# Kernel tuning notes

Measured on AMD Instinct MI355X. Metric: run time of the kernel, lower is better.

The kernel has to match this reference:

```python
import jax, jax.numpy as jnp
import numpy as np

B, L, C, H = 4, 4096, 1024, 16


def setup_inputs() -> dict:
    key = jax.random.key(0)
    k1, k2, k3 = jax.random.split(key, 3)
    x = jax.random.normal(k1, (B, L, C), dtype=jnp.float32)
    # torch nn.Linear params: weight (out, in), bias (out,)
    W_qkv = jax.random.normal(k2, (3 * C, C), dtype=jnp.float32) * 0.02
    b_qkv = jnp.zeros((3 * C,), dtype=jnp.float32)
    W_out = jax.random.normal(k3, (C, C), dtype=jnp.float32) * 0.02
    b_out = jnp.zeros((C,), dtype=jnp.float32)
    return {"x": x, "W_qkv": W_qkv, "b_qkv": b_qkv, "W_out": W_out,
            "b_out": b_out, "num_heads": H}


def reference(x, W_qkv, b_qkv, W_out, b_out, num_heads):
    # Faithful to the source, INCLUDING its head-axis bug:
    # q,k,v stay (B, L, H, D); attention is computed over the HEAD axis
    # (H x H per token), and the final transpose(1,2).reshape scrambles
    # sequence/head layout exactly as torch does.
    b, l, c = x.shape
    h = num_heads
    d = c // h
    scale = d ** (-0.5)
    qkv = (x @ W_qkv.T + b_qkv).reshape(b, l, 3, h, d)
    q, k, v = qkv[:, :, 0], qkv[:, :, 1], qkv[:, :, 2]  # (B, L, H, D)
    # (B,L,H,D) @ (B,L,D,H) -> (B,L,H,H)
    attn = jnp.einsum('blhd,blgd->blhg', q, k) * scale
    attn = jax.nn.softmax(attn, axis=-1)
    # dropout is identity in eval mode
    out = jnp.einsum('blhg,blgd->blhd', attn, v)      # (B, L, H, D)
    out = jnp.swapaxes(out, 1, 2).reshape(b, l, c)    # torch transpose(1,2).reshape
    return out @ W_out.T + b_out
```

## Files before the change

kernel.cpp:

```cpp
#include <hip/hip_runtime.h>
#include <hip/hip_bf16.h>


typedef __attribute__((ext_vector_type(8))) short bf16x8;
typedef __attribute__((ext_vector_type(4))) float f32x4;

__device__ __forceinline__ float bf2f(unsigned short u) {
    union { unsigned int i; float f; } x;
    x.i = ((unsigned int)u) << 16;
    return x.f;
}
__device__ __forceinline__ unsigned short f2bf(float f) {
    unsigned int u = __float_as_uint(f);
    u = (u + 0x7FFFu + ((u >> 16) & 1u)) >> 16;
    return (unsigned short)u;
}

#define VMCNT4() asm volatile("s_waitcnt vmcnt(4)" ::: "memory")
#define VMCNT0() asm volatile("s_waitcnt vmcnt(0)" ::: "memory")
#define LGKM0()  asm volatile("s_waitcnt lgkmcnt(0)" ::: "memory")
#define BAR()    __builtin_amdgcn_s_barrier()

__global__ __launch_bounds__(256) void cast_all(const float* __restrict__ x,
                                                const float* __restrict__ wq,
                                                const float* __restrict__ wo,
                                                unsigned short* __restrict__ xb,
                                                unsigned short* __restrict__ wqb,
                                                unsigned short* __restrict__ wob) {
    const size_t base = (size_t)blockIdx.x * 2048 + threadIdx.x;
#pragma unroll
    for (int it = 0; it < 8; ++it) {
        size_t i = base + (size_t)it * 256;
        const float4* s; ushort4* d; size_t off;
        if (i < 4194304)      { s = (const float4*)x;  d = (ushort4*)xb;  off = i; }
        else if (i < 4980736) { s = (const float4*)wq; d = (ushort4*)wqb; off = i - 4194304; }
        else                  { s = (const float4*)wo; d = (ushort4*)wob; off = i - 4980736; }
        float4 v = s[off];
        ushort4 o;
        o.x = f2bf(v.x); o.y = f2bf(v.y); o.z = f2bf(v.z); o.w = f2bf(v.w);
        d[off] = o;
    }
}

template<int OUTF32>
__global__ __launch_bounds__(512, 2) void gemm256(const unsigned short* __restrict__ A,
                                                  const unsigned short* __restrict__ B,
                                                  const float* __restrict__ bias,
                                                  unsigned short* __restrict__ Cb,
                                                  float* __restrict__ Cf,
                                                  int M, int N, int K, int NXT) {
    __shared__ __align__(16) unsigned short lds[2][2][2][8192];

    const int tid  = threadIdx.x;
    const int lane = tid & 63;
    const int wave = tid >> 6;
    const int wr = wave >> 2;
    const int wc = wave & 3;
    const int fr = lane & 15;
    const int fq = lane >> 4;
    const int frx = fr & 7;

    const int nwg  = gridDim.x;
    const int orig = blockIdx.x;
    const int wg   = (orig & 7) * (nwg >> 3) + (orig >> 3);
    const int tileM = (wg / NXT) * 256;
    const int tileN = (wg % NXT) * 256;

    const int r8  = tid >> 3;
    const int jsw = (tid & 7) ^ (r8 & 7);
    const unsigned short* Ap = A;
    const unsigned short* Bp = B;

#define STAGE(nb, OPp, HH, ktt) do {                                                   \
    const unsigned short* gb = (OPp) ? Bp : Ap;                                        \
    const int rb = ((OPp) ? tileN : tileM) + (HH) * 128 + r8;                          \
    const unsigned short* s0 = gb + (size_t)rb * K + (ktt) * 64 + jsw * 8;             \
    unsigned short* d0 = &lds[nb][OPp][HH][tid * 8];                                   \
    __builtin_amdgcn_global_load_lds((const __attribute__((address_space(1))) void*)s0,\
        (__attribute__((address_space(3))) void*)d0, 16, 0, 0);                        \
    __builtin_amdgcn_global_load_lds(                                                  \
        (const __attribute__((address_space(1))) void*)(s0 + (size_t)64 * K),          \
        (__attribute__((address_space(3))) void*)(d0 + 4096), 16, 0, 0);               \
} while (0)

#define READ_A(h) do {                                                                 \
    _Pragma("unroll") for (int i2 = 0; i2 < 4; ++i2) {                                 \
        const int ar = (wr * 64 + i2 * 16 + fr) * 64;                                  \
        af[i2][0] = *(const bf16x8*)&lds[cur][0][h][ar + ((fq ^ frx) << 3)];           \
        af[i2][1] = *(const bf16x8*)&lds[cur][0][h][ar + (((4 + fq) ^ frx) << 3)];     \
    }                                                                                  \
} while (0)

#define READ_B(g) do {                                                                 \
    _Pragma("unroll") for (int j2 = 0; j2 < 2; ++j2) {                                 \
        const int br = (wc * 32 + j2 * 16 + fr) * 64;                                  \
        bfr[2*(g)+j2][0] = *(const bf16x8*)&lds[cur][1][g][br + ((fq ^ frx) << 3)];    \
        bfr[2*(g)+j2][1] = *(const bf16x8*)&lds[cur][1][g][br + (((4 + fq) ^ frx) << 3)];\
    }                                                                                  \
} while (0)

#define MFMA_Q(h, g) do {                                                              \
    __builtin_amdgcn_s_setprio(1);                                                     \
    _Pragma("unroll") for (int i2 = 0; i2 < 4; ++i2)                                   \
    _Pragma("unroll") for (int j2 = 0; j2 < 2; ++j2) {                                 \
        acc[(h)*4+i2][(g)*2+j2] = __builtin_amdgcn_mfma_f32_16x16x32_bf16(             \
            af[i2][0], bfr[2*(g)+j2][0], acc[(h)*4+i2][(g)*2+j2], 0, 0, 0);            \
        acc[(h)*4+i2][(g)*2+j2] = __builtin_amdgcn_mfma_f32_16x16x32_bf16(             \
            af[i2][1], bfr[2*(g)+j2][1], acc[(h)*4+i2][(g)*2+j2], 0, 0, 0);            \
    }                                                                                  \
    __builtin_amdgcn_s_setprio(0);                                                     \
} while (0)

    f32x4 acc[8][4];
#pragma unroll
    for (int i = 0; i < 8; ++i)
#pragma unroll
        for (int j = 0; j < 4; ++j) acc[i][j] = (f32x4){0.f, 0.f, 0.f, 0.f};

    STAGE(0, 0, 0, 0);
    STAGE(0, 1, 0, 0);
    STAGE(0, 1, 1, 0);
    STAGE(0, 0, 1, 0);
    VMCNT4();
    BAR();

    const int NT = K >> 6;
    int cur = 0;
    for (int kt = 0; kt < NT - 1; ++kt) {
        const int nb = cur ^ 1;
        bf16x8 af[4][2], bfr[4][2];
        READ_A(0); READ_B(0); STAGE(nb, 0, 0, kt + 1); VMCNT4(); BAR(); LGKM0(); MFMA_Q(0, 0);
        READ_B(1); STAGE(nb, 1, 0, kt + 1); VMCNT4(); BAR(); LGKM0(); MFMA_Q(0, 1);
        READ_A(1); STAGE(nb, 1, 1, kt + 1); BAR(); LGKM0(); MFMA_Q(1, 0);
        STAGE(nb, 0, 1, kt + 1); VMCNT4(); BAR(); MFMA_Q(1, 1);
        cur = nb;
    }
    VMCNT0();
    BAR();
    {
        bf16x8 af[4][2], bfr[4][2];
        READ_A(0); READ_B(0); LGKM0(); MFMA_Q(0, 0);
        READ_B(1);            LGKM0(); MFMA_Q(0, 1);
        READ_A(1);            LGKM0(); MFMA_Q(1, 0);
                                       MFMA_Q(1, 1);
    }

#pragma unroll
    for (int i = 0; i < 8; ++i) {
        const int row = tileM + (i >> 2) * 128 + wr * 64 + (i & 3) * 16 + fq * 4;
#pragma unroll
        for (int j = 0; j < 4; ++j) {
            const int col = tileN + (j >> 1) * 128 + wc * 32 + (j & 1) * 16 + fr;
            const float bv = bias[col];
#pragma unroll
            for (int r = 0; r < 4; ++r) {
                const float v = acc[i][j][r] + bv;
                if (OUTF32) Cf[(size_t)(row + r) * N + col] = v;
                else        Cb[(size_t)(row + r) * N + col] = f2bf(v);
            }
        }
    }
#undef STAGE
#undef READ_A
#undef READ_B
#undef MFMA_Q
}

__global__ __launch_bounds__(256) void attn_kernel(const unsigned short* __restrict__ qkv,
                                                   unsigned short* __restrict__ scr) {
    __shared__ __align__(16) unsigned short sbuf[4][3072];
    __shared__ float Pl[4][256];

    const int wave = threadIdx.x >> 6, lane = threadIdx.x & 63;
    const int token = blockIdx.x * 4 + wave;
    const int b = token >> 12, l = token & 4095;

    const unsigned short* src = qkv + (size_t)token * 3072;
#pragma unroll
    for (int i = 0; i < 6; ++i) {
        int off = (i * 64 + lane) * 8;
        *(bf16x8*)&sbuf[wave][off] = *(const bf16x8*)&src[off];
    }
    __syncthreads();

    const unsigned short* sq = sbuf[wave];

    float sv[4];
#pragma unroll
    for (int r = 0; r < 4; ++r) {
        const int p = r * 64 + lane;
        const int h = p >> 4, g = p & 15;
        float acc = 0.f;
#pragma unroll
        for (int d8 = 0; d8 < 8; ++d8) {
            bf16x8 qa = *(const bf16x8*)&sq[h * 64 + d8 * 8];
            bf16x8 kb = *(const bf16x8*)&sq[1024 + g * 64 + d8 * 8];
#pragma unroll
            for (int j = 0; j < 8; ++j)
                acc += bf2f((unsigned short)qa[j]) * bf2f((unsigned short)kb[j]);
        }
        sv[r] = acc * 0.125f;
    }

#pragma unroll
    for (int r = 0; r < 4; ++r) {
        float m = sv[r];
        m = fmaxf(m, __shfl_xor(m, 1));
        m = fmaxf(m, __shfl_xor(m, 2));
        m = fmaxf(m, __shfl_xor(m, 4));
        m = fmaxf(m, __shfl_xor(m, 8));
        float e = __expf(sv[r] - m);
        float s = e;
        s += __shfl_xor(s, 1);
        s += __shfl_xor(s, 2);
        s += __shfl_xor(s, 4);
        s += __shfl_xor(s, 8);
        Pl[wave][r * 64 + lane] = e / s;
    }
    __syncthreads();

    float vreg[16];
#pragma unroll
    for (int g = 0; g < 16; ++g) vreg[g] = bf2f(sq[2048 + g * 64 + lane]);

    const int q_ = l >> 4, j = l & 15;
    const size_t base = ((size_t)b * 4096 + q_) * 1024 + j * 64 + lane;
#pragma unroll
    for (int h = 0; h < 16; ++h) {
        float acc = 0.f;
#pragma unroll
        for (int g = 0; g < 16; ++g) acc += Pl[wave][h * 16 + g] * vreg[g];
        scr[base + (size_t)h * 256 * 1024] = f2bf(acc);
    }
}

extern "C" void kernel_launch(void* const* d_in, const int* in_sizes, int n_in,
                              void* d_out, int out_size, void* d_ws, size_t ws_size,
                              hipStream_t stream) {
    const float* x    = (const float*)d_in[0];
    const float* Wqkv = (const float*)d_in[1];
    const float* bqkv = (const float*)d_in[2];
    const float* Wout = (const float*)d_in[3];
    const float* bout = (const float*)d_in[4];
    float* out = (float*)d_out;

    char* ws = (char*)d_ws;
    unsigned short* xb   = (unsigned short*)(ws);
    unsigned short* wqb  = (unsigned short*)(ws + 33554432);
    unsigned short* wob  = (unsigned short*)(ws + 39845888);
    unsigned short* qkvb = (unsigned short*)(ws + 41943040);
    unsigned short* scr  = (unsigned short*)(ws + 142606336);

    cast_all<<<2560, 256, 0, stream>>>(x, Wqkv, Wout, xb, wqb, wob);

    gemm256<0><<<768, 512, 0, stream>>>(xb, wqb, bqkv, qkvb, nullptr, 16384, 3072, 1024, 12);

    attn_kernel<<<4096, 256, 0, stream>>>(qkvb, scr);

    gemm256<1><<<256, 512, 0, stream>>>(scr, wob, bout, nullptr, out, 16384, 1024, 1024, 4);
}
```

Measured before the change: 197.8 us.

## Make QKV GEMM persistent over N tiles with continuous k-loop prefetch

The QKV GEMM now launches 256 workgroups instead of 768, each computing three consecutive 256-wide N tiles for its M tile. The k-loop runs across tile boundaries, so the next tile's first k-slab is prefetched while the current tile finishes. The epilogue is written mid-loop. This is meant to remove the pipeline drain and refill at each tile boundary and to avoid a partial second wave of workgroups on the 256-CU device. In exchange, the epilogue stores now sit inside the main loop and can stall it, and the tile-to-workgroup mapping is hardcoded to four N groups per M tile.

```diff
diff --git a/kernel.cpp b/kernel.cpp
--- a/kernel.cpp
+++ b/kernel.cpp
@@ -42,13 +42,13 @@
     }
 }
 
-template<int OUTF32>
+template<int OUTF32, int NTILES>
 __global__ __launch_bounds__(512, 2) void gemm256(const unsigned short* __restrict__ A,
                                                   const unsigned short* __restrict__ B,
                                                   const float* __restrict__ bias,
                                                   unsigned short* __restrict__ Cb,
                                                   float* __restrict__ Cf,
-                                                  int M, int N, int K, int NXT) {
+                                                  int N, int K) {
     __shared__ __align__(16) unsigned short lds[2][2][2][8192];
 
     const int tid  = threadIdx.x;
@@ -63,19 +63,19 @@
     const int nwg  = gridDim.x;
     const int orig = blockIdx.x;
     const int wg   = (orig & 7) * (nwg >> 3) + (orig >> 3);
-    const int tileM = (wg / NXT) * 256;
-    const int tileN = (wg % NXT) * 256;
+    const int tileM = (wg >> 2) * 256;
+    const int n0    = (wg & 3) * NTILES;
 
     const int r8  = tid >> 3;
     const int jsw = (tid & 7) ^ (r8 & 7);
     const unsigned short* Ap = A;
     const unsigned short* Bp = B;
 
-#define STAGE(nb, OPp, HH, ktt) do {                                                   \
+#define STAGE(nbuf, OPp, HH, base, ktt) do {                                           \
     const unsigned short* gb = (OPp) ? Bp : Ap;                                        \
-    const int rb = ((OPp) ? tileN : tileM) + (HH) * 128 + r8;                          \
+    const int rb = (base) + (HH) * 128 + r8;                                           \
     const unsigned short* s0 = gb + (size_t)rb * K + (ktt) * 64 + jsw * 8;             \
-    unsigned short* d0 = &lds[nb][OPp][HH][tid * 8];                                   \
+    unsigned short* d0 = &lds[nbuf][OPp][HH][tid * 8];                                 \
     __builtin_amdgcn_global_load_lds((const __attribute__((address_space(1))) void*)s0,\
         (__attribute__((address_space(3))) void*)d0, 16, 0, 0);                        \
     __builtin_amdgcn_global_load_lds(                                                  \
@@ -111,59 +111,75 @@
     __builtin_amdgcn_s_setprio(0);                                                     \
 } while (0)
 
+#define EPILOGUE(tn) do {                                                              \
+    _Pragma("unroll") for (int i = 0; i < 8; ++i) {                                    \
+        const int row = tileM + (i >> 2) * 128 + wr * 64 + (i & 3) * 16 + fq * 4;      \
+        _Pragma("unroll") for (int j = 0; j < 4; ++j) {                                \
+            const int col = (tn) + (j >> 1) * 128 + wc * 32 + (j & 1) * 16 + fr;       \
+            const float bv = bias[col];                                                \
+            _Pragma("unroll") for (int r = 0; r < 4; ++r) {                            \
+                const float v = acc[i][j][r] + bv;                                     \
+                if (OUTF32) Cf[(size_t)(row + r) * N + col] = v;                       \
+                else        Cb[(size_t)(row + r) * N + col] = f2bf(v);                 \
+            }                                                                          \
+        }                                                                              \
+    }                                                                                  \
+    _Pragma("unroll") for (int i = 0; i < 8; ++i)                                      \
+    _Pragma("unroll") for (int j = 0; j < 4; ++j) acc[i][j] = (f32x4){0.f,0.f,0.f,0.f};\
+} while (0)
+
     f32x4 acc[8][4];
 #pragma unroll
     for (int i = 0; i < 8; ++i)
 #pragma unroll
         for (int j = 0; j < 4; ++j) acc[i][j] = (f32x4){0.f, 0.f, 0.f, 0.f};
 
-    STAGE(0, 0, 0, 0);
-    STAGE(0, 1, 0, 0);
-    STAGE(0, 1, 1, 0);
-    STAGE(0, 0, 1, 0);
+    const int NT    = K >> 6;
+    const int NITER = NTILES * NT;
+
+    {
+        const int tN0 = n0 * 256;
+        STAGE(0, 0, 0, tileM, 0);
+        STAGE(0, 1, 0, tN0,   0);
+        STAGE(0, 1, 1, tN0,   0);
+        STAGE(0, 0, 1, tileM, 0);
+    }
     VMCNT4();
     BAR();
 
-    const int NT = K >> 6;
-    int cur = 0;
-    for (int kt = 0; kt < NT - 1; ++kt) {
-        const int nb = cur ^ 1;
+    int kk  = 0;
+    int tNc = n0 * 256;
+    for (int it = 0; it < NITER - 1; ++it) {
+        const int cur = it & 1, nb = cur ^ 1;
+        int kk2 = kk + 1, tN2 = tNc;
+        if (kk2 == NT) { kk2 = 0; tN2 += 256; }
         bf16x8 af[4][2], bfr[4][2];
-        READ_A(0); READ_B(0); STAGE(nb, 0, 0, kt + 1); VMCNT4(); BAR(); LGKM0(); MFMA_Q(0, 0);
-        READ_B(1); STAGE(nb, 1, 0, kt + 1); VMCNT4(); BAR(); LGKM0(); MFMA_Q(0, 1);
-        READ_A(1); STAGE(nb, 1, 1, kt + 1); BAR(); LGKM0(); MFMA_Q(1, 0);
-        STAGE(nb, 0, 1, kt + 1); VMCNT4(); BAR(); MFMA_Q(1, 1);
-        cur = nb;
+        READ_A(0); READ_B(0); STAGE(nb, 0, 0, tileM, kk2); VMCNT4(); BAR(); LGKM0(); MFMA_Q(0, 0);
+        READ_B(1);            STAGE(nb, 1, 0, tN2,   kk2); VMCNT4(); BAR(); LGKM0(); MFMA_Q(0, 1);
+        READ_A(1);            STAGE(nb, 1, 1, tN2,   kk2);           BAR(); LGKM0(); MFMA_Q(1, 0);
+                              STAGE(nb, 0, 1, tileM, kk2); VMCNT4(); BAR();          MFMA_Q(1, 1);
+        if (kk2 == 0) {
+            EPILOGUE(tNc);
+            tNc += 256;
+        }
+        kk = kk2;
     }
     VMCNT0();
     BAR();
     {
+        const int cur = (NITER - 1) & 1;
         bf16x8 af[4][2], bfr[4][2];
         READ_A(0); READ_B(0); LGKM0(); MFMA_Q(0, 0);
         READ_B(1);            LGKM0(); MFMA_Q(0, 1);
         READ_A(1);            LGKM0(); MFMA_Q(1, 0);
                                        MFMA_Q(1, 1);
     }
-
-#pragma unroll
-    for (int i = 0; i < 8; ++i) {
-        const int row = tileM + (i >> 2) * 128 + wr * 64 + (i & 3) * 16 + fq * 4;
-#pragma unroll
-        for (int j = 0; j < 4; ++j) {
-            const int col = tileN + (j >> 1) * 128 + wc * 32 + (j & 1) * 16 + fr;
-            const float bv = bias[col];
-#pragma unroll
-            for (int r = 0; r < 4; ++r) {
-                const float v = acc[i][j][r] + bv;
-                if (OUTF32) Cf[(size_t)(row + r) * N + col] = v;
-                else        Cb[(size_t)(row + r) * N + col] = f2bf(v);
-            }
-        }
-    }
+    EPILOGUE(tNc);
 #undef STAGE
 #undef READ_A
 #undef READ_B
 #undef MFMA_Q
+#undef EPILOGUE
 }
 
 __global__ __launch_bounds__(256) void attn_kernel(const unsigned short* __restrict__ qkv,
@@ -253,9 +269,9 @@
 
     cast_all<<<2560, 256, 0, stream>>>(x, Wqkv, Wout, xb, wqb, wob);
 
-    gemm256<0><<<768, 512, 0, stream>>>(xb, wqb, bqkv, qkvb, nullptr, 16384, 3072, 1024, 12);
+    gemm256<0, 3><<<256, 512, 0, stream>>>(xb, wqb, bqkv, qkvb, nullptr, 3072, 1024);
 
     attn_kernel<<<4096, 256, 0, stream>>>(qkvb, scr);
 
-    gemm256<1><<<256, 512, 0, stream>>>(scr, wob, bout, nullptr, out, 16384, 1024, 1024, 4);
-}
+    gemm256<1, 1><<<256, 512, 0, stream>>>(scr, wob, bout, nullptr, out, 1024, 1024);
+}
```

Result: slower. 211.6 us (+7.0%).
